# Performance work log

Measured on AMD Instinct MI355X. Metric: run time of the kernel, lower is better.

Reference implementation:

```python
import jax, jax.numpy as jnp
import numpy as np

N_HEAD = 16
N_EMBD = 1024

def setup_inputs() -> dict:
    key = jax.random.key(0)
    ks = jax.random.split(key, 7)
    B, S, D = 2, 2048, N_EMBD
    scale = 1.0 / np.sqrt(D)
    return {
        "x": jax.random.normal(ks[0], (B, S, D), dtype=jnp.float32),
        "Wq": jax.random.normal(ks[1], (D, D), dtype=jnp.float32) * scale,
        "bq": jnp.zeros((D,), dtype=jnp.float32),
        "Wk": jax.random.normal(ks[2], (D, D), dtype=jnp.float32) * scale,
        "bk": jnp.zeros((D,), dtype=jnp.float32),
        "Wv": jax.random.normal(ks[3], (D, D), dtype=jnp.float32) * scale,
        "bv": jnp.zeros((D,), dtype=jnp.float32),
    }

def reference(x, Wq, bq, Wk, bk, Wv, bv):
    B, S, D = x.shape
    H = N_HEAD
    hd = D // H
    # QKV projections
    q = (x @ Wq + bq).reshape(B, S, H, hd).transpose(0, 2, 1, 3)  # [B,H,S,hd]
    k = (x @ Wk + bk).reshape(B, S, H, hd).transpose(0, 2, 1, 3)
    v = (x @ Wv + bv).reshape(B, S, H, hd).transpose(0, 2, 1, 3)
    # Note: original module defines a causal mask but never applies it.
    att = jnp.einsum("bhqd,bhkd->bhqk", q, k) * (1.0 / jnp.sqrt(hd).astype(x.dtype))
    att = jax.nn.softmax(att, axis=-1)
    y = jnp.einsum("bhqk,bhkd->bhqd", att, v)  # [B,H,S,hd]
    return y.transpose(0, 2, 1, 3).reshape(B, S, D)
```

## Files before the change

kernel.cpp:

```cpp
#include <hip/hip_runtime.h>


#define D_MODEL 1024
#define NHEAD   16
#define HDIM    64
#define SEQ     2048
#define MROWS   4096

typedef __attribute__((ext_vector_type(8))) short short8;
typedef __attribute__((ext_vector_type(4))) float f32x4;

__device__ __forceinline__ float bf2f(unsigned short u) {
  return __uint_as_float(((unsigned int)u) << 16);
}
__device__ __forceinline__ unsigned short f2bf(float f) {
  unsigned int u = __float_as_uint(f);
  u += 0x7fff + ((u >> 16) & 1);
  return (unsigned short)(u >> 16);
}

__device__ __forceinline__ int sniff_bf16(const unsigned short* x) {
  int cnt = 0;
#pragma unroll
  for (int i = 0; i < 64; ++i) {
    const unsigned e = (x[2 * i] >> 7) & 0xFF;
    cnt += (e >= 105 && e <= 140) ? 1 : 0;
  }
  return cnt >= 48;
}

__device__ __forceinline__ void gl_lds16(const unsigned short* g, unsigned short* l) {
  __builtin_amdgcn_global_load_lds(
      (const __attribute__((address_space(1))) unsigned int*)g,
      (__attribute__((address_space(3))) unsigned int*)l, 16, 0, 0);
}

__global__ __launch_bounds__(256) void cvt_x(const unsigned short* __restrict__ X,
                                             unsigned short* __restrict__ Xbf) {
  const int isbf = sniff_bf16(X);
  const size_t i0 = ((size_t)blockIdx.x * 256 + threadIdx.x) * 8;
  if (isbf) {
    *(uint4*)(Xbf + i0) = *(const uint4*)(X + i0);
  } else {
    const float* Xf = (const float*)X;
    const float4 f0 = *(const float4*)(Xf + i0);
    const float4 f1 = *(const float4*)(Xf + i0 + 4);
    unsigned short t[8] = {f2bf(f0.x), f2bf(f0.y), f2bf(f0.z), f2bf(f0.w),
                           f2bf(f1.x), f2bf(f1.y), f2bf(f1.z), f2bf(f1.w)};
    *(uint4*)(Xbf + i0) = *(const uint4*)t;
  }
}

__global__ __launch_bounds__(256) void cvt_w(
    const unsigned short* __restrict__ w0, const unsigned short* __restrict__ w1,
    const unsigned short* __restrict__ w2,
    const unsigned short* __restrict__ b0, const unsigned short* __restrict__ b1,
    const unsigned short* __restrict__ b2,
    unsigned short* __restrict__ Wt, unsigned short* __restrict__ bb) {
  __shared__ unsigned short tile[32][33];
  const int z = blockIdx.z;
  const unsigned short* W    = (z == 0) ? w0 : ((z == 1) ? w1 : w2);
  const unsigned short* bias = (z == 0) ? b0 : ((z == 1) ? b1 : b2);
  unsigned short* Wtz = Wt + ((size_t)z << 20);
  const int isbf = sniff_bf16(W);
  const int bx = blockIdx.x * 32;
  const int by = blockIdx.y * 32;
  const int tx = threadIdx.x & 31;
  const int ty = threadIdx.x >> 5;
#pragma unroll
  for (int r = ty; r < 32; r += 8) {
    unsigned short v;
    if (isbf) v = W[(size_t)(by + r) * D_MODEL + bx + tx];
    else      v = f2bf(((const float*)W)[(size_t)(by + r) * D_MODEL + bx + tx]);
    tile[r][tx] = v;
  }
  __syncthreads();
#pragma unroll
  for (int r = ty; r < 32; r += 8)
    Wtz[(size_t)(bx + r) * D_MODEL + by + tx] = tile[tx][r];
  if (blockIdx.x == 0 && blockIdx.y == 0) {
    const int i0 = threadIdx.x * 4;
#pragma unroll
    for (int j = 0; j < 4; ++j)
      bb[z * D_MODEL + i0 + j] =
          isbf ? bias[i0 + j] : f2bf(((const float*)bias)[i0 + j]);
  }
}

__device__ __forceinline__ void store_cd(int z, unsigned short* Out, int row0,
                                         int col, const f32x4 acc, float bb) {
  if (z == 2) {
    const int b = row0 >> 11, s = row0 & 2047;
    const int bh = b * NHEAD + (col >> 6);
    ushort4 pk;
    pk.x = f2bf(acc[0] + bb); pk.y = f2bf(acc[1] + bb);
    pk.z = f2bf(acc[2] + bb); pk.w = f2bf(acc[3] + bb);
    *(ushort4*)(Out + ((size_t)bh * HDIM + (col & 63)) * SEQ + s) = pk;
  } else {
#pragma unroll
    for (int r = 0; r < 4; ++r)
      Out[(size_t)(row0 + r) * D_MODEL + col] = f2bf(acc[r] + bb);
  }
}

__global__ __launch_bounds__(256) void qkv_gemm_fast(
    const unsigned short* __restrict__ Xbf, const unsigned short* __restrict__ Wt,
    const unsigned short* __restrict__ bb,
    unsigned short* __restrict__ Oq, unsigned short* __restrict__ Ok,
    unsigned short* __restrict__ Ov) {
  const int z = blockIdx.z;
  const unsigned short* Wz = Wt + ((size_t)z << 20);
  unsigned short* Out = (z == 0) ? Oq : ((z == 1) ? Ok : Ov);

  __shared__ unsigned short As[128 * 32];
  __shared__ unsigned short Bs[128 * 32];

  const int tid  = threadIdx.x;
  const int wave = tid >> 6, lane = tid & 63;
  const int wm = wave >> 1, wn = wave & 1;
  const int lrow = lane & 15, lk = lane >> 4;
  const int m0 = blockIdx.y * 128;
  const int n0 = blockIdx.x * 128;

  f32x4 acc[4][4] = {};

  for (int kk = 0; kk < D_MODEL; kk += 32) {
#pragma unroll
    for (int i = 0; i < 2; ++i) {
      const int c = i * 256 + tid;
      const int row = c >> 2, off = (c & 3) * 8;
      gl_lds16(Xbf + (size_t)(m0 + row) * D_MODEL + kk + off, &As[c * 8]);
      gl_lds16(Wz  + (size_t)(n0 + row) * D_MODEL + kk + off, &Bs[c * 8]);
    }
    __syncthreads();
    short8 a[4], b[4];
#pragma unroll
    for (int t = 0; t < 4; ++t) {
      a[t] = *(const short8*)(&As[(wm * 64 + t * 16 + lrow) * 32 + lk * 8]);
      b[t] = *(const short8*)(&Bs[(wn * 64 + t * 16 + lrow) * 32 + lk * 8]);
    }
#pragma unroll
    for (int mt = 0; mt < 4; ++mt)
#pragma unroll
      for (int nt = 0; nt < 4; ++nt)
        acc[mt][nt] = __builtin_amdgcn_mfma_f32_16x16x32_bf16(a[mt], b[nt], acc[mt][nt], 0, 0, 0);
    __syncthreads();
  }
#pragma unroll
  for (int nt = 0; nt < 4; ++nt) {
    const int col = n0 + wn * 64 + nt * 16 + lrow;
    const float bv = bf2f(bb[z * D_MODEL + col]);
#pragma unroll
    for (int mt = 0; mt < 4; ++mt)
      store_cd(z, Out, m0 + wm * 64 + mt * 16 + lk * 4, col, acc[mt][nt], bv);
  }
}

#define LDA 40
__global__ __launch_bounds__(256) void qkv_gemm_med(
    const unsigned short* __restrict__ X, const unsigned short* __restrict__ Wt,
    const unsigned short* __restrict__ bb,
    unsigned short* __restrict__ Oq, unsigned short* __restrict__ Ok,
    unsigned short* __restrict__ Ov) {
  const int z = blockIdx.z;
  const unsigned short* Wz = Wt + ((size_t)z << 20);
  unsigned short* Out = (z == 0) ? Oq : ((z == 1) ? Ok : Ov);

  __shared__ alignas(16) unsigned short As[128 * LDA];
  __shared__ alignas(16) unsigned short Bs[128 * LDA];

  const int isbf = sniff_bf16(X);
  const int tid  = threadIdx.x;
  const int wave = tid >> 6, lane = tid & 63;
  const int wm = wave >> 1, wn = wave & 1;
  const int lrow = lane & 15, lk = lane >> 4;
  const int m0 = blockIdx.y * 128;
  const int n0 = blockIdx.x * 128;

  f32x4 acc[4][4] = {};

  for (int kk = 0; kk < D_MODEL; kk += 32) {
#pragma unroll
    for (int i = 0; i < 2; ++i) {
      const int c = tid + i * 256;
      const int row = c >> 2, off = (c & 3) * 8;
      if (isbf) {
        *(uint4*)(&As[row * LDA + off]) =
            *(const uint4*)(X + (size_t)(m0 + row) * D_MODEL + kk + off);
      } else {
        const float* Xf = (const float*)X;
        const float4 f0 = *(const float4*)(Xf + (size_t)(m0 + row) * D_MODEL + kk + off);
        const float4 f1 = *(const float4*)(Xf + (size_t)(m0 + row) * D_MODEL + kk + off + 4);
        unsigned short t[8] = {f2bf(f0.x), f2bf(f0.y), f2bf(f0.z), f2bf(f0.w),
                               f2bf(f1.x), f2bf(f1.y), f2bf(f1.z), f2bf(f1.w)};
        *(uint4*)(&As[row * LDA + off]) = *(const uint4*)t;
      }
      *(uint4*)(&Bs[row * LDA + off]) =
          *(const uint4*)(Wz + (size_t)(n0 + row) * D_MODEL + kk + off);
    }
    __syncthreads();
    short8 a[4], b[4];
#pragma unroll
    for (int t = 0; t < 4; ++t) {
      a[t] = *(const short8*)(&As[(wm * 64 + t * 16 + lrow) * LDA + lk * 8]);
      b[t] = *(const short8*)(&Bs[(wn * 64 + t * 16 + lrow) * LDA + lk * 8]);
    }
#pragma unroll
    for (int mt = 0; mt < 4; ++mt)
#pragma unroll
      for (int nt = 0; nt < 4; ++nt)
        acc[mt][nt] = __builtin_amdgcn_mfma_f32_16x16x32_bf16(a[mt], b[nt], acc[mt][nt], 0, 0, 0);
    __syncthreads();
  }
#pragma unroll
  for (int nt = 0; nt < 4; ++nt) {
    const int col = n0 + wn * 64 + nt * 16 + lrow;
    const float bv = bf2f(bb[z * D_MODEL + col]);
#pragma unroll
    for (int mt = 0; mt < 4; ++mt)
      store_cd(z, Out, m0 + wm * 64 + mt * 16 + lk * 4, col, acc[mt][nt], bv);
  }
}

__global__ __launch_bounds__(256) void qkv_gemm(
    const unsigned short* __restrict__ X,
    const unsigned short* __restrict__ Wq, const unsigned short* __restrict__ Wk,
    const unsigned short* __restrict__ Wv,
    const unsigned short* __restrict__ bq, const unsigned short* __restrict__ bk,
    const unsigned short* __restrict__ bv,
    unsigned short* __restrict__ Oq, unsigned short* __restrict__ Ok,
    unsigned short* __restrict__ Ov) {
  const int z = blockIdx.z;
  const unsigned short* W    = (z == 0) ? Wq : ((z == 1) ? Wk : Wv);
  const unsigned short* bias = (z == 0) ? bq : ((z == 1) ? bk : bv);
  unsigned short*       Out  = (z == 0) ? Oq : ((z == 1) ? Ok : Ov);

  __shared__ alignas(16) unsigned short As[128 * LDA];
  __shared__ alignas(16) unsigned short Bs[128 * LDA];

  const int isbf = sniff_bf16(X);
  const int tid  = threadIdx.x;
  const int wave = tid >> 6, lane = tid & 63;
  const int wm = wave >> 1, wn = wave & 1;
  const int lrow = lane & 15, lk = lane >> 4;
  const int m0 = blockIdx.y * 128;
  const int n0 = blockIdx.x * 128;

  f32x4 acc[4][4] = {};

  for (int kk = 0; kk < D_MODEL; kk += 32) {
#pragma unroll
    for (int i = 0; i < 2; ++i) {
      const int c = tid + i * 256;
      const int row = c >> 2, off = (c & 3) * 8;
      if (isbf) {
        *(uint4*)(&As[row * LDA + off]) =
            *(const uint4*)(X + (size_t)(m0 + row) * D_MODEL + kk + off);
      } else {
        const float* Xf = (const float*)X;
        const float4 f0 = *(const float4*)(Xf + (size_t)(m0 + row) * D_MODEL + kk + off);
        const float4 f1 = *(const float4*)(Xf + (size_t)(m0 + row) * D_MODEL + kk + off + 4);
        unsigned short t[8] = {f2bf(f0.x), f2bf(f0.y), f2bf(f0.z), f2bf(f0.w),
                               f2bf(f1.x), f2bf(f1.y), f2bf(f1.z), f2bf(f1.w)};
        *(uint4*)(&As[row * LDA + off]) = *(const uint4*)t;
      }
    }
#pragma unroll
    for (int i = 0; i < 2; ++i) {
      const int c = tid + i * 256;
      const int krow = c & 31;
      const int nc0 = (c >> 5) * 8;
      if (isbf) {
        uint4 v = *(const uint4*)(W + (size_t)(kk + krow) * D_MODEL + n0 + nc0);
        const unsigned short* e = (const unsigned short*)&v;
#pragma unroll
        for (int j = 0; j < 8; ++j) Bs[(nc0 + j) * LDA + krow] = e[j];
      } else {
        const float* Wf = (const float*)W;
        const float4 f0 = *(const float4*)(Wf + (size_t)(kk + krow) * D_MODEL + n0 + nc0);
        const float4 f1 = *(const float4*)(Wf + (size_t)(kk + krow) * D_MODEL + n0 + nc0 + 4);
        const float vals[8] = {f0.x, f0.y, f0.z, f0.w, f1.x, f1.y, f1.z, f1.w};
#pragma unroll
        for (int j = 0; j < 8; ++j) Bs[(nc0 + j) * LDA + krow] = f2bf(vals[j]);
      }
    }
    __syncthreads();
    short8 a[4], b[4];
#pragma unroll
    for (int t = 0; t < 4; ++t) {
      a[t] = *(const short8*)(&As[(wm * 64 + t * 16 + lrow) * LDA + lk * 8]);
      b[t] = *(const short8*)(&Bs[(wn * 64 + t * 16 + lrow) * LDA + lk * 8]);
    }
#pragma unroll
    for (int mt = 0; mt < 4; ++mt)
#pragma unroll
      for (int nt = 0; nt < 4; ++nt)
        acc[mt][nt] = __builtin_amdgcn_mfma_f32_16x16x32_bf16(a[mt], b[nt], acc[mt][nt], 0, 0, 0);
    __syncthreads();
  }
#pragma unroll
  for (int nt = 0; nt < 4; ++nt) {
    const int col = n0 + wn * 64 + nt * 16 + lrow;
    const float bv2 = isbf ? bf2f(bias[col]) : ((const float*)bias)[col];
#pragma unroll
    for (int mt = 0; mt < 4; ++mt)
      store_cd(z, Out, m0 + wm * 64 + mt * 16 + lk * 4, col, acc[mt][nt], bv2);
  }
}

#define LDK 72
__global__ __launch_bounds__(256) void attn(
    const unsigned short* __restrict__ Qg, const unsigned short* __restrict__ Kg,
    const unsigned short* __restrict__ Vtg, unsigned short* __restrict__ Outg,
    const unsigned short* __restrict__ Xs) {
  const int qt = blockIdx.x;
  const int bh = blockIdx.y;
  const int b = bh >> 4, h = bh & 15;
  const size_t baseR = (size_t)b * SEQ * D_MODEL + h * HDIM;
  const size_t baseV = (size_t)bh * HDIM * SEQ;

  __shared__ alignas(16) unsigned short Ks[64 * LDK];
  __shared__ alignas(16) unsigned short Vs[64 * LDK];
  __shared__ alignas(16) unsigned short Ps[128 * LDK];

  const int isbf = sniff_bf16(Xs);
  const int tid  = threadIdx.x;
  const int wave = tid >> 6, lane = tid & 63;
  const int lrow = lane & 15, lk = lane >> 4;
  const int q0 = qt * 128;
  const int wq = wave * 32;

  short8 qf[2][2];
#pragma unroll
  for (int nq = 0; nq < 2; ++nq)
#pragma unroll
    for (int ks = 0; ks < 2; ++ks)
      qf[nq][ks] = *(const short8*)(Qg + baseR +
          (size_t)(q0 + wq + nq * 16 + lrow) * D_MODEL + ks * 32 + lk * 8);

  f32x4 accO[2][4] = {};
  float lsum[2] = {0.f, 0.f};
  const float csc = 0.18033688011112042f;

  for (int kv0 = 0; kv0 < SEQ; kv0 += 64) {
    __syncthreads();
#pragma unroll
    for (int i = 0; i < 2; ++i) {
      const int c = tid + i * 256;
      const int row = c >> 3, off = (c & 7) * 8;
      *(uint4*)(&Ks[row * LDK + off]) =
          *(const uint4*)(Kg + baseR + (size_t)(kv0 + row) * D_MODEL + off);
      *(uint4*)(&Vs[row * LDK + off]) =
          *(const uint4*)(Vtg + baseV + (size_t)row * SEQ + kv0 + off);
    }
    __syncthreads();

    f32x4 accST[4][2] = {};
#pragma unroll
    for (int ks = 0; ks < 2; ++ks) {
      short8 kf[4];
#pragma unroll
      for (int mt = 0; mt < 4; ++mt)
        kf[mt] = *(const short8*)(&Ks[(mt * 16 + lrow) * LDK + ks * 32 + lk * 8]);
#pragma unroll
      for (int mt = 0; mt < 4; ++mt)
#pragma unroll
        for (int nq = 0; nq < 2; ++nq)
          accST[mt][nq] = __builtin_amdgcn_mfma_f32_16x16x32_bf16(
              kf[mt], qf[nq][ks], accST[mt][nq], 0, 0, 0);
    }

#pragma unroll
    for (int mt = 0; mt < 4; ++mt)
#pragma unroll
      for (int nq = 0; nq < 2; ++nq) {
        float p0 = exp2f(accST[mt][nq][0] * csc), p1 = exp2f(accST[mt][nq][1] * csc);
        float p2 = exp2f(accST[mt][nq][2] * csc), p3 = exp2f(accST[mt][nq][3] * csc);
        lsum[nq] += (p0 + p1) + (p2 + p3);
        ushort4 pk = {f2bf(p0), f2bf(p1), f2bf(p2), f2bf(p3)};
        *(ushort4*)(&Ps[(wq + nq * 16 + lrow) * LDK + mt * 16 + lk * 4]) = pk;
      }

#pragma unroll
    for (int ks = 0; ks < 2; ++ks) {
      short8 pf[2], vf[4];
#pragma unroll
      for (int mq = 0; mq < 2; ++mq)
        pf[mq] = *(const short8*)(&Ps[(wq + mq * 16 + lrow) * LDK + ks * 32 + lk * 8]);
#pragma unroll
      for (int nd = 0; nd < 4; ++nd)
        vf[nd] = *(const short8*)(&Vs[(nd * 16 + lrow) * LDK + ks * 32 + lk * 8]);
#pragma unroll
      for (int mq = 0; mq < 2; ++mq)
#pragma unroll
        for (int nd = 0; nd < 4; ++nd)
          accO[mq][nd] = __builtin_amdgcn_mfma_f32_16x16x32_bf16(
              pf[mq], vf[nd], accO[mq][nd], 0, 0, 0);
    }
  }

#pragma unroll
  for (int nq = 0; nq < 2; ++nq) {
    lsum[nq] += __shfl_xor(lsum[nq], 16, 64);
    lsum[nq] += __shfl_xor(lsum[nq], 32, 64);
  }
  __syncthreads();
  float* Lf = (float*)Ps;
  if (lk == 0) {
    Lf[wq + lrow]      = lsum[0];
    Lf[wq + 16 + lrow] = lsum[1];
  }
#pragma unroll
  for (int mq = 0; mq < 2; ++mq) {
    const f32x4 l4 = *(const f32x4*)(&Lf[wq + mq * 16 + lk * 4]);
#pragma unroll
    for (int r = 0; r < 4; ++r) {
      const float inv = 1.0f / l4[r];
      const int row = q0 + wq + mq * 16 + lk * 4 + r;
#pragma unroll
      for (int nd = 0; nd < 4; ++nd) {
        const int col = h * HDIM + nd * 16 + lrow;
        const float val = accO[mq][nd][r] * inv;
        const size_t idx = (size_t)b * SEQ * D_MODEL + (size_t)row * D_MODEL + col;
        if (isbf) Outg[idx] = f2bf(val);
        else      ((float*)Outg)[idx] = val;
      }
    }
  }
}

extern "C" void kernel_launch(void* const* d_in, const int* in_sizes, int n_in,
                              void* d_out, int out_size, void* d_ws, size_t ws_size,
                              hipStream_t stream) {
  const unsigned short* x  = (const unsigned short*)d_in[0];
  const unsigned short* Wq = (const unsigned short*)d_in[1];
  const unsigned short* bq = (const unsigned short*)d_in[2];
  const unsigned short* Wk = (const unsigned short*)d_in[3];
  const unsigned short* bk = (const unsigned short*)d_in[4];
  const unsigned short* Wv = (const unsigned short*)d_in[5];
  const unsigned short* bv = (const unsigned short*)d_in[6];
  unsigned short* out = (unsigned short*)d_out;
  unsigned short* ws  = (unsigned short*)d_ws;

  const size_t M1 = 1u << 20;
  const size_t wsE = ws_size / 2;

  unsigned short* Wt  = ws;
  unsigned short* bb  = ws + 3 * M1;
  unsigned short* K   = ws + 3 * M1 + 65536;
  unsigned short* Vt  = K + 4 * M1;
  unsigned short* Xbf = Vt + 4 * M1;
  unsigned short* Q;

  if (wsE >= 19 * M1 + 65536) {
    Q = Xbf + 4 * M1;
    cvt_x<<<dim3(2048), 256, 0, stream>>>(x, Xbf);
    cvt_w<<<dim3(32, 32, 3), 256, 0, stream>>>(Wq, Wk, Wv, bq, bk, bv, Wt, bb);
    qkv_gemm_fast<<<dim3(8, 32, 3), 256, 0, stream>>>(Xbf, Wt, bb, Q, K, Vt);
  } else if (wsE >= 15 * M1 + 65536) {
    Q = out;
    cvt_x<<<dim3(2048), 256, 0, stream>>>(x, Xbf);
    cvt_w<<<dim3(32, 32, 3), 256, 0, stream>>>(Wq, Wk, Wv, bq, bk, bv, Wt, bb);
    qkv_gemm_fast<<<dim3(8, 32, 3), 256, 0, stream>>>(Xbf, Wt, bb, Q, K, Vt);
  } else if (wsE >= 11 * M1 + 65536) {
    Q = out;
    cvt_w<<<dim3(32, 32, 3), 256, 0, stream>>>(Wq, Wk, Wv, bq, bk, bv, Wt, bb);
    qkv_gemm_med<<<dim3(8, 32, 3), 256, 0, stream>>>(x, Wt, bb, Q, K, Vt);
  } else {
    if (wsE >= 12 * M1) { Q = ws; K = ws + 4 * M1; Vt = ws + 8 * M1; }
    else                { Q = out; K = ws; Vt = ws + 4 * M1; }
    qkv_gemm<<<dim3(8, 32, 3), 256, 0, stream>>>(x, Wq, Wk, Wv, bq, bk, bv, Q, K, Vt);
  }
  attn<<<dim3(16, 32), 256, 0, stream>>>(Q, K, Vt, out, x);
}
```

Baseline: 229.6 us.

## Prefetch K/V tiles into registers, fold softmax scale into Q, use packed bf16 cvt

The attention loop now loads the next K/V tile from global memory into registers while the current tile is being computed, then writes it to LDS after a barrier, so load latency overlaps the MFMA work. The softmax scale (log2e/sqrt(hd)) is folded into the Q projection epilogue, which removes a multiply before every exp2. Float-to-bf16 conversions in several places switch to the hardware v_cvt_pk_bf16_f32 instruction. This raises register pressure from the prefetch buffers and changes where Q is rounded relative to the scale.

```diff
diff --git a/kernel.cpp b/kernel.cpp
--- a/kernel.cpp
+++ b/kernel.cpp
@@ -6,6 +6,7 @@
 #define HDIM    64
 #define SEQ     2048
 #define MROWS   4096
+#define CSC     0.18033688011112042f
 
 typedef __attribute__((ext_vector_type(8))) short short8;
 typedef __attribute__((ext_vector_type(4))) float f32x4;
@@ -17,6 +18,11 @@
   unsigned int u = __float_as_uint(f);
   u += 0x7fff + ((u >> 16) & 1);
   return (unsigned short)(u >> 16);
+}
+__device__ __forceinline__ unsigned int cvtpk_bf16(float lo, float hi) {
+  unsigned int r;
+  asm("v_cvt_pk_bf16_f32 %0, %1, %2" : "=v"(r) : "v"(lo), "v"(hi));
+  return r;
 }
 
 __device__ __forceinline__ int sniff_bf16(const unsigned short* x) {
@@ -45,8 +51,8 @@
     const float* Xf = (const float*)X;
     const float4 f0 = *(const float4*)(Xf + i0);
     const float4 f1 = *(const float4*)(Xf + i0 + 4);
-    unsigned short t[8] = {f2bf(f0.x), f2bf(f0.y), f2bf(f0.z), f2bf(f0.w),
-                           f2bf(f1.x), f2bf(f1.y), f2bf(f1.z), f2bf(f1.w)};
+    unsigned int t[4] = {cvtpk_bf16(f0.x, f0.y), cvtpk_bf16(f0.z, f0.w),
+                         cvtpk_bf16(f1.x, f1.y), cvtpk_bf16(f1.z, f1.w)};
     *(uint4*)(Xbf + i0) = *(const uint4*)t;
   }
 }
@@ -88,18 +94,19 @@
 }
 
 __device__ __forceinline__ void store_cd(int z, unsigned short* Out, int row0,
-                                         int col, const f32x4 acc, float bb) {
+                                         int col, const f32x4 acc, float bb,
+                                         float sc) {
   if (z == 2) {
     const int b = row0 >> 11, s = row0 & 2047;
     const int bh = b * NHEAD + (col >> 6);
-    ushort4 pk;
-    pk.x = f2bf(acc[0] + bb); pk.y = f2bf(acc[1] + bb);
-    pk.z = f2bf(acc[2] + bb); pk.w = f2bf(acc[3] + bb);
-    *(ushort4*)(Out + ((size_t)bh * HDIM + (col & 63)) * SEQ + s) = pk;
+    uint2 pk;
+    pk.x = cvtpk_bf16(acc[0] + bb, acc[1] + bb);
+    pk.y = cvtpk_bf16(acc[2] + bb, acc[3] + bb);
+    *(uint2*)(Out + ((size_t)bh * HDIM + (col & 63)) * SEQ + s) = pk;
   } else {
 #pragma unroll
     for (int r = 0; r < 4; ++r)
-      Out[(size_t)(row0 + r) * D_MODEL + col] = f2bf(acc[r] + bb);
+      Out[(size_t)(row0 + r) * D_MODEL + col] = f2bf((acc[r] + bb) * sc);
   }
 }
 
@@ -111,6 +118,7 @@
   const int z = blockIdx.z;
   const unsigned short* Wz = Wt + ((size_t)z << 20);
   unsigned short* Out = (z == 0) ? Oq : ((z == 1) ? Ok : Ov);
+  const float sc = (z == 0) ? CSC : 1.0f;
 
   __shared__ unsigned short As[128 * 32];
   __shared__ unsigned short Bs[128 * 32];
@@ -152,7 +160,7 @@
     const float bv = bf2f(bb[z * D_MODEL + col]);
 #pragma unroll
     for (int mt = 0; mt < 4; ++mt)
-      store_cd(z, Out, m0 + wm * 64 + mt * 16 + lk * 4, col, acc[mt][nt], bv);
+      store_cd(z, Out, m0 + wm * 64 + mt * 16 + lk * 4, col, acc[mt][nt], bv, sc);
   }
 }
 
@@ -165,6 +173,7 @@
   const int z = blockIdx.z;
   const unsigned short* Wz = Wt + ((size_t)z << 20);
   unsigned short* Out = (z == 0) ? Oq : ((z == 1) ? Ok : Ov);
+  const float sc = (z == 0) ? CSC : 1.0f;
 
   __shared__ alignas(16) unsigned short As[128 * LDA];
   __shared__ alignas(16) unsigned short Bs[128 * LDA];
@@ -191,8 +200,8 @@
         const float* Xf = (const float*)X;
         const float4 f0 = *(const float4*)(Xf + (size_t)(m0 + row) * D_MODEL + kk + off);
         const float4 f1 = *(const float4*)(Xf + (size_t)(m0 + row) * D_MODEL + kk + off + 4);
-        unsigned short t[8] = {f2bf(f0.x), f2bf(f0.y), f2bf(f0.z), f2bf(f0.w),
-                               f2bf(f1.x), f2bf(f1.y), f2bf(f1.z), f2bf(f1.w)};
+        unsigned int t[4] = {cvtpk_bf16(f0.x, f0.y), cvtpk_bf16(f0.z, f0.w),
+                             cvtpk_bf16(f1.x, f1.y), cvtpk_bf16(f1.z, f1.w)};
         *(uint4*)(&As[row * LDA + off]) = *(const uint4*)t;
       }
       *(uint4*)(&Bs[row * LDA + off]) =
@@ -218,7 +227,7 @@
     const float bv = bf2f(bb[z * D_MODEL + col]);
 #pragma unroll
     for (int mt = 0; mt < 4; ++mt)
-      store_cd(z, Out, m0 + wm * 64 + mt * 16 + lk * 4, col, acc[mt][nt], bv);
+      store_cd(z, Out, m0 + wm * 64 + mt * 16 + lk * 4, col, acc[mt][nt], bv, sc);
   }
 }
 
@@ -234,6 +243,7 @@
   const unsigned short* W    = (z == 0) ? Wq : ((z == 1) ? Wk : Wv);
   const unsigned short* bias = (z == 0) ? bq : ((z == 1) ? bk : bv);
   unsigned short*       Out  = (z == 0) ? Oq : ((z == 1) ? Ok : Ov);
+  const float sc = (z == 0) ? CSC : 1.0f;
 
   __shared__ alignas(16) unsigned short As[128 * LDA];
   __shared__ alignas(16) unsigned short Bs[128 * LDA];
@@ -260,8 +270,8 @@
         const float* Xf = (const float*)X;
         const float4 f0 = *(const float4*)(Xf + (size_t)(m0 + row) * D_MODEL + kk + off);
         const float4 f1 = *(const float4*)(Xf + (size_t)(m0 + row) * D_MODEL + kk + off + 4);
-        unsigned short t[8] = {f2bf(f0.x), f2bf(f0.y), f2bf(f0.z), f2bf(f0.w),
-                               f2bf(f1.x), f2bf(f1.y), f2bf(f1.z), f2bf(f1.w)};
+        unsigned int t[4] = {cvtpk_bf16(f0.x, f0.y), cvtpk_bf16(f0.z, f0.w),
+                             cvtpk_bf16(f1.x, f1.y), cvtpk_bf16(f1.z, f1.w)};
         *(uint4*)(&As[row * LDA + off]) = *(const uint4*)t;
       }
     }
@@ -304,7 +314,7 @@
     const float bv2 = isbf ? bf2f(bias[col]) : ((const float*)bias)[col];
 #pragma unroll
     for (int mt = 0; mt < 4; ++mt)
-      store_cd(z, Out, m0 + wm * 64 + mt * 16 + lk * 4, col, acc[mt][nt], bv2);
+      store_cd(z, Out, m0 + wm * 64 + mt * 16 + lk * 4, col, acc[mt][nt], bv2, sc);
   }
 }
 
@@ -340,20 +350,35 @@
 
   f32x4 accO[2][4] = {};
   float lsum[2] = {0.f, 0.f};
-  const float csc = 0.18033688011112042f;
-
-  for (int kv0 = 0; kv0 < SEQ; kv0 += 64) {
-    __syncthreads();
+
+  uint4 kreg[2], vreg[2];
+  auto LOADT = [&](int kv) {
 #pragma unroll
     for (int i = 0; i < 2; ++i) {
       const int c = tid + i * 256;
       const int row = c >> 3, off = (c & 7) * 8;
-      *(uint4*)(&Ks[row * LDK + off]) =
-          *(const uint4*)(Kg + baseR + (size_t)(kv0 + row) * D_MODEL + off);
-      *(uint4*)(&Vs[row * LDK + off]) =
-          *(const uint4*)(Vtg + baseV + (size_t)row * SEQ + kv0 + off);
-    }
-    __syncthreads();
+      kreg[i] = *(const uint4*)(Kg + baseR + (size_t)(kv + row) * D_MODEL + off);
+      vreg[i] = *(const uint4*)(Vtg + baseV + (size_t)row * SEQ + kv + off);
+    }
+  };
+  auto WRITET = [&]() {
+#pragma unroll
+    for (int i = 0; i < 2; ++i) {
+      const int c = tid + i * 256;
+      const int row = c >> 3, off = (c & 7) * 8;
+      *(uint4*)(&Ks[row * LDK + off]) = kreg[i];
+      *(uint4*)(&Vs[row * LDK + off]) = vreg[i];
+    }
+  };
+
+  LOADT(0);
+  WRITET();
+  __syncthreads();
+
+#pragma unroll 1
+  for (int kv0 = 0; kv0 < SEQ; kv0 += 64) {
+    const int nxt = kv0 + 64;
+    if (nxt < SEQ) LOADT(nxt);
 
     f32x4 accST[4][2] = {};
 #pragma unroll
@@ -374,11 +399,13 @@
     for (int mt = 0; mt < 4; ++mt)
 #pragma unroll
       for (int nq = 0; nq < 2; ++nq) {
-        float p0 = exp2f(accST[mt][nq][0] * csc), p1 = exp2f(accST[mt][nq][1] * csc);
-        float p2 = exp2f(accST[mt][nq][2] * csc), p3 = exp2f(accST[mt][nq][3] * csc);
+        const float p0 = exp2f(accST[mt][nq][0]), p1 = exp2f(accST[mt][nq][1]);
+        const float p2 = exp2f(accST[mt][nq][2]), p3 = exp2f(accST[mt][nq][3]);
         lsum[nq] += (p0 + p1) + (p2 + p3);
-        ushort4 pk = {f2bf(p0), f2bf(p1), f2bf(p2), f2bf(p3)};
-        *(ushort4*)(&Ps[(wq + nq * 16 + lrow) * LDK + mt * 16 + lk * 4]) = pk;
+        uint2 pk;
+        pk.x = cvtpk_bf16(p0, p1);
+        pk.y = cvtpk_bf16(p2, p3);
+        *(uint2*)(&Ps[(wq + nq * 16 + lrow) * LDK + mt * 16 + lk * 4]) = pk;
       }
 
 #pragma unroll
@@ -397,6 +424,10 @@
           accO[mq][nd] = __builtin_amdgcn_mfma_f32_16x16x32_bf16(
               pf[mq], vf[nd], accO[mq][nd], 0, 0, 0);
     }
+
+    __syncthreads();
+    if (nxt < SEQ) WRITET();
+    __syncthreads();
   }
 
 #pragma unroll
```

Result: no change. 227.4 us (-1.0%).
